# Performance work log

Hardware: AMD Instinct MI355X
Metric: run time of the kernel (lower is better)

Reference implementation:

```python
import jax, jax.numpy as jnp
import numpy as np

LAMBDA_BOX = 1.0
LAMBDA_OBJ = 1.0
IOU_THRESHOLD = 0.2
ALPHA = 0.25
GAMMA = 2.0
EPS = 1e-7  # torchvision complete_box_iou_loss eps


def box_cxcywh_to_xyxy(boxes):
    # boxes [..., 4] (cx, cy, w, h); w,h clamped to min 1e-4 as in the torch code
    cx, cy, w, h = jnp.split(boxes, 4, axis=-1)
    w = jnp.maximum(w, 1e-4)
    h = jnp.maximum(h, 1e-4)
    return jnp.concatenate([cx - w / 2, cy - h / 2, cx + w / 2, cy + h / 2], axis=-1)


def pairwise_box_iou(a, b):
    # a [B,N,4] xyxy, b [B,M,4] xyxy -> [B,N,M] (torchvision box_iou: inter/union, no eps)
    a = a[:, :, None, :]  # [B,N,1,4]
    b = b[:, None, :, :]  # [B,1,M,4]
    lt = jnp.maximum(a[..., :2], b[..., :2])
    rb = jnp.minimum(a[..., 2:], b[..., 2:])
    wh = jnp.clip(rb - lt, 0.0)
    inter = wh[..., 0] * wh[..., 1]
    area_a = (a[..., 2] - a[..., 0]) * (a[..., 3] - a[..., 1])
    area_b = (b[..., 2] - b[..., 0]) * (b[..., 3] - b[..., 1])
    return inter / (area_a + area_b - inter)


def ciou_loss(p, t):
    # torchvision.ops.complete_box_iou_loss, elementwise over [...,4] xyxy boxes
    x1p, y1p, x2p, y2p = p[..., 0], p[..., 1], p[..., 2], p[..., 3]
    x1t, y1t, x2t, y2t = t[..., 0], t[..., 1], t[..., 2], t[..., 3]
    lt_x = jnp.maximum(x1p, x1t); lt_y = jnp.maximum(y1p, y1t)
    rb_x = jnp.minimum(x2p, x2t); rb_y = jnp.minimum(y2p, y2t)
    inter = jnp.clip(rb_x - lt_x, 0.0) * jnp.clip(rb_y - lt_y, 0.0)
    union = (x2p - x1p) * (y2p - y1p) + (x2t - x1t) * (y2t - y1t) - inter
    iou = inter / (union + EPS)
    # smallest enclosing box diagonal
    cx1 = jnp.minimum(x1p, x1t); cy1 = jnp.minimum(y1p, y1t)
    cx2 = jnp.maximum(x2p, x2t); cy2 = jnp.maximum(y2p, y2t)
    diag = (cx2 - cx1) ** 2 + (cy2 - cy1) ** 2 + EPS
    centers = ((x1p + x2p - x1t - x2t) ** 2 + (y1p + y2p - y1t - y2t) ** 2) / 4.0
    diou = 1.0 - iou + centers / diag
    wp = x2p - x1p; hp = y2p - y1p
    wt = x2t - x1t; ht = y2t - y1t
    v = (4.0 / (jnp.pi ** 2)) * (jnp.arctan(wt / ht) - jnp.arctan(wp / hp)) ** 2
    alpha = jax.lax.stop_gradient(v / (1.0 - iou + v + EPS))
    return diou + alpha * v


def focal_loss_mean(logits, targets):
    # mean over last axis; matches torch focal_loss with alpha=0.25, gamma=2
    prob = jax.nn.sigmoid(logits)
    # stable BCE-with-logits
    ce = jnp.clip(logits, 0.0) - logits * targets + jnp.log1p(jnp.exp(-jnp.abs(logits)))
    p_t = prob * targets + (1.0 - prob) * (1.0 - targets)
    alpha_t = ALPHA * targets + (1.0 - ALPHA) * (1.0 - targets)
    p_t = jnp.clip(p_t, 1e-6, 1.0 - 1e-6)
    return (alpha_t * (1.0 - p_t) ** GAMMA * ce).mean(axis=-1)


def greedy_match(iou_nm):
    # iou_nm [N,M]: sequential greedy per-GT matching with conf_target gating
    N = iou_nm.shape[0]
    def step(conf_t, iou_col):
        best = jnp.argmax(iou_col)
        ok = (iou_col[best] > IOU_THRESHOLD) & (conf_t[best] < 0.01)
        conf_t = jnp.where(ok, conf_t.at[best].set(1.0), conf_t)
        return conf_t, (best, ok)
    conf_target, (idx, mask) = jax.lax.scan(step, jnp.zeros((N,), iou_nm.dtype), iou_nm.T)
    return conf_target, idx, mask


def setup_inputs() -> dict:
    key = jax.random.key(0)
    k1, k2, k3, k4, k5 = jax.random.split(key, 5)
    B, N, M = 16, 25000, 64
    # predictions: cx,cy in [0,1], w,h in [0.02,0.3], conf logit ~ N(0,1)
    pcxy = jax.random.uniform(k1, (B, N, 2), jnp.float32)
    pwh = jax.random.uniform(k2, (B, N, 2), jnp.float32, 0.02, 0.3)
    pconf = jax.random.normal(k3, (B, N, 1), jnp.float32)
    preds = jnp.concatenate([pcxy, pwh, pconf], axis=-1)
    # GT boxes in xyxy (as consumed directly by box_iou in the torch code)
    gcxy = jax.random.uniform(k4, (B, M, 2), jnp.float32)
    gwh = jax.random.uniform(k5, (B, M, 2), jnp.float32, 0.02, 0.3)
    targets = box_cxcywh_to_xyxy(jnp.concatenate([gcxy, gwh], axis=-1))
    return {"preds": preds, "targets": targets}


def reference(preds, targets):
    # preds [B,N,5], targets [B,M,4] xyxy -> scalar loss
    pred_xyxy = box_cxcywh_to_xyxy(preds[..., :4])  # [B,N,4]
    pred_conf = preds[..., 4]                        # [B,N]
    # matching indices are non-differentiable (argmax selection)
    iou_m = pairwise_box_iou(jax.lax.stop_gradient(pred_xyxy),
                             jax.lax.stop_gradient(targets))  # [B,N,M]
    conf_target, idx, mask = jax.vmap(greedy_match)(iou_m)  # [B,N], [B,M], [B,M]
    conf_loss = focal_loss_mean(pred_conf, conf_target)      # [B]
    # gather matched pred boxes and compute masked-mean CIoU loss per image
    pb = jnp.take_along_axis(pred_xyxy, idx[..., None], axis=1)  # [B,M,4]
    ciou = ciou_loss(pb, targets)                                # [B,M]
    m = mask.astype(ciou.dtype)
    n_match = m.sum(axis=1)
    box_loss = (ciou * m).sum(axis=1) / jnp.maximum(n_match, 1.0)
    per_image = LAMBDA_OBJ * conf_loss + jnp.where(n_match > 0, LAMBDA_BOX * box_loss, 0.0)
    return per_image.mean()
```

## Files before the change

kernel.cpp:

```cpp
#include <hip/hip_runtime.h>
#include <math.h>

#define BATCH 16
#define NPRED 25000
#define MTGT  64
#define CHUNKS 32
#define PPC   800
#define ABLK  512
#define WAVES (ABLK / 64)
#define PPW   (PPC / WAVES)

#define GMAX_OFF 256
#define WS_ZERO_BYTES (GMAX_OFF + BATCH * MTGT * 8)

__device__ __forceinline__ float focal_term(float x, float t) {
    float prob = 1.0f / (1.0f + expf(-x));
    float ce = fmaxf(x, 0.0f) - x * t + log1pf(expf(-fabsf(x)));
    float p_t = prob * t + (1.0f - prob) * (1.0f - t);
    float alpha_t = 0.25f * t + 0.75f * (1.0f - t);
    p_t = fminf(fmaxf(p_t, 1e-6f), 1.0f - 1e-6f);
    float om = 1.0f - p_t;
    return alpha_t * om * om * ce;
}

__global__ __launch_bounds__(ABLK) void iou_argmax_kernel(
    const float* __restrict__ preds,
    const float* __restrict__ targets,
    unsigned long long* __restrict__ gmax,
    float* __restrict__ focal0)
{
    const int b = blockIdx.y;
    const int chunk = blockIdx.x;
    const int t = threadIdx.x;
    const int lane = t & 63;
    const int w = t >> 6;

    __shared__ float4 sbox[PPC];
    __shared__ unsigned long long comb[WAVES][MTGT];
    __shared__ float sfocal[WAVES];

    float fsum = 0.0f;
    for (int idx = t; idx < PPC; idx += ABLK) {
        int n = chunk * PPC + idx;
        float4 bx;
        if (n < NPRED) {
            const float* p = preds + ((long)b * NPRED + n) * 5;
            float cx = p[0], cy = p[1];
            float wd = fmaxf(p[2], 1e-4f);
            float hh = fmaxf(p[3], 1e-4f);
            bx.x = cx - wd / 2.0f;
            bx.y = cy - hh / 2.0f;
            bx.z = cx + wd / 2.0f;
            bx.w = cy + hh / 2.0f;
            fsum += focal_term(p[4], 0.0f);
        } else {
            bx = make_float4(3e8f, 3e8f, 3e8f, 3e8f);
        }
        sbox[idx] = bx;
    }
    for (int off = 32; off > 0; off >>= 1) fsum += __shfl_down(fsum, off);
    if (lane == 0) sfocal[w] = fsum;

    const float* tg = targets + ((long)b * MTGT + lane) * 4;
    float tx1 = tg[0], ty1 = tg[1], tx2 = tg[2], ty2 = tg[3];
    float ta = (tx2 - tx1) * (ty2 - ty1);

    __syncthreads();

    const int nbase = chunk * PPC + w * PPW;
    float best_i = 0.0f, best_d = 1.0f;
    int best_n = nbase;
#pragma unroll 4
    for (int j = 0; j < PPW; j++) {
        float4 bx = sbox[w * PPW + j];
        float ap = (bx.z - bx.x) * (bx.w - bx.y);
        float ltx = fmaxf(bx.x, tx1), lty = fmaxf(bx.y, ty1);
        float rbx = fminf(bx.z, tx2), rby = fminf(bx.w, ty2);
        float inter = fmaxf(rbx - ltx, 0.0f) * fmaxf(rby - lty, 0.0f);
        float den = ap + ta - inter;
        bool better = (inter * best_d) > (best_i * den);
        best_i = better ? inter : best_i;
        best_d = better ? den : best_d;
        best_n = better ? (nbase + j) : best_n;
    }
    float iou = best_i / best_d;
    comb[w][lane] =
        ((unsigned long long)__float_as_uint(iou) << 32) | (unsigned int)(~best_n);

    __syncthreads();

    if (t < MTGT) {
        unsigned long long v = comb[0][t];
        for (int ww = 1; ww < WAVES; ww++) {
            unsigned long long o = comb[ww][t];
            v = (o > v) ? o : v;
        }
        atomicMax(&gmax[b * MTGT + t], v);
    }
    if (t == 0) {
        float s = 0.0f;
        for (int ww = 0; ww < WAVES; ww++) s += sfocal[ww];
        atomicAdd(&focal0[b], s);
    }
}

__global__ __launch_bounds__(64) void finalize_kernel(
    const float* __restrict__ preds,
    const float* __restrict__ targets,
    const unsigned long long* __restrict__ gmax,
    const float* __restrict__ focal0,
    float* __restrict__ out)
{
    const int b = blockIdx.x;
    const int t = threadIdx.x;

    unsigned long long packed = gmax[b * MTGT + t];
    int id = (int)(~(unsigned int)packed);

    const float* tgp = targets + ((long)b * MTGT + t) * 4;
    float x1t = tgp[0], y1t = tgp[1], x2t = tgp[2], y2t = tgp[3];

    float x1p = 0.f, y1p = 0.f, x2p = 0.f, y2p = 0.f, cf = 0.f;
    float v = 0.0f;
    if (id >= 0 && id < NPRED) {
        const float* p = preds + ((long)b * NPRED + id) * 5;
        float cx = p[0], cy = p[1];
        float wd = fmaxf(p[2], 1e-4f);
        float hh = fmaxf(p[3], 1e-4f);
        cf = p[4];
        x1p = cx - wd / 2.0f; y1p = cy - hh / 2.0f;
        x2p = cx + wd / 2.0f; y2p = cy + hh / 2.0f;
        float ltx = fmaxf(x1p, x1t), lty = fmaxf(y1p, y1t);
        float rbx = fminf(x2p, x2t), rby = fminf(y2p, y2t);
        float inter = fmaxf(rbx - ltx, 0.0f) * fmaxf(rby - lty, 0.0f);
        float ap = (x2p - x1p) * (y2p - y1p);
        float at = (x2t - x1t) * (y2t - y1t);
        v = inter / (ap + at - inter);
    }

    bool accepted = false;
    for (int m = 0; m < MTGT; m++) {
        float vm = __shfl(v, m);
        int im = __shfl(id, m);
        unsigned long long conflict = __ballot(accepted && (id == im));
        bool ok = (vm > 0.2f) && (conflict == 0ull);
        if (t == m) accepted = ok;
    }

    float csum = 0.0f, dsum = 0.0f;
    int cnt = 0;
    if (accepted) {
        float ltx = fmaxf(x1p, x1t), lty = fmaxf(y1p, y1t);
        float rbx = fminf(x2p, x2t), rby = fminf(y2p, y2t);
        float inter = fmaxf(rbx - ltx, 0.0f) * fmaxf(rby - lty, 0.0f);
        float uni = (x2p - x1p) * (y2p - y1p) + (x2t - x1t) * (y2t - y1t) - inter;
        float iou = inter / (uni + 1e-7f);
        float cx1 = fminf(x1p, x1t), cy1 = fminf(y1p, y1t);
        float cx2 = fmaxf(x2p, x2t), cy2 = fmaxf(y2p, y2t);
        float dx = cx2 - cx1, dy = cy2 - cy1;
        float diag = dx * dx + dy * dy + 1e-7f;
        float ex = x1p + x2p - x1t - x2t;
        float ey = y1p + y2p - y1t - y2t;
        float centers = (ex * ex + ey * ey) / 4.0f;
        float diou = 1.0f - iou + centers / diag;
        float wp = x2p - x1p, hp = y2p - y1p;
        float wt = x2t - x1t, ht = y2t - y1t;
        float dat = atanf(wt / ht) - atanf(wp / hp);
        float vv = 0.40528473f * (dat * dat);
        float alpha = vv / (1.0f - iou + vv + 1e-7f);
        csum = diou + alpha * vv;
        cnt = 1;
        dsum = focal_term(cf, 1.0f) - focal_term(cf, 0.0f);
    }

    for (int off = 32; off > 0; off >>= 1) {
        csum += __shfl_down(csum, off);
        dsum += __shfl_down(dsum, off);
        cnt  += __shfl_down(cnt, off);
    }
    if (t == 0) {
        float conf = (focal0[b] + dsum) / (float)NPRED;
        float per = conf;
        if (cnt > 0) per += csum / (float)cnt;
        atomicAdd(out, per * (1.0f / (float)BATCH));
    }
}

extern "C" void kernel_launch(void* const* d_in, const int* in_sizes, int n_in,
                              void* d_out, int out_size, void* d_ws, size_t ws_size,
                              hipStream_t stream) {
    const float* preds = (const float*)d_in[0];
    const float* targets = (const float*)d_in[1];
    float* out = (float*)d_out;

    float* focal0 = (float*)d_ws;
    unsigned long long* gmax = (unsigned long long*)((char*)d_ws + GMAX_OFF);

    hipMemsetAsync(d_out, 0, sizeof(float), stream);
    hipMemsetAsync(d_ws, 0, WS_ZERO_BYTES, stream);

    dim3 gridA(CHUNKS, BATCH);
    iou_argmax_kernel<<<gridA, ABLK, 0, stream>>>(preds, targets, gmax, focal0);
    finalize_kernel<<<BATCH, 64, 0, stream>>>(preds, targets, gmax, focal0, out);
}
```

Before: 87.69 us.

## Replace atomics and memsets with per-chunk partials reduced in single-block finalize

The first kernel now writes per-chunk argmax and focal partial results to the workspace instead of using atomicMax/atomicAdd, so both hipMemsetAsync calls can be removed. The finalize kernel becomes one 1024-thread block that reduces the partials per image and writes the output directly. Chunks are doubled to 64 of 400 predictions each, giving 1024 blocks for more parallelism. The inner IoU loop is also restructured to compare two boxes per step, which shortens the dependent compare chain. In exchange, finalize reads more partial data and all batch work runs on a single block.

```diff
diff --git a/kernel.cpp b/kernel.cpp
--- a/kernel.cpp
+++ b/kernel.cpp
@@ -4,14 +4,13 @@
 #define BATCH 16
 #define NPRED 25000
 #define MTGT  64
-#define CHUNKS 32
-#define PPC   800
+#define CHUNKS 64
+#define PPC   400
 #define ABLK  512
 #define WAVES (ABLK / 64)
 #define PPW   (PPC / WAVES)
 
-#define GMAX_OFF 256
-#define WS_ZERO_BYTES (GMAX_OFF + BATCH * MTGT * 8)
+#define PART_BYTES ((size_t)BATCH * CHUNKS * MTGT * 8)
 
 __device__ __forceinline__ float focal_term(float x, float t) {
     float prob = 1.0f / (1.0f + expf(-x));
@@ -26,8 +25,8 @@
 __global__ __launch_bounds__(ABLK) void iou_argmax_kernel(
     const float* __restrict__ preds,
     const float* __restrict__ targets,
-    unsigned long long* __restrict__ gmax,
-    float* __restrict__ focal0)
+    unsigned long long* __restrict__ part,
+    float* __restrict__ focalp)
 {
     const int b = blockIdx.y;
     const int chunk = blockIdx.x;
@@ -40,8 +39,8 @@
     __shared__ float sfocal[WAVES];
 
     float fsum = 0.0f;
-    for (int idx = t; idx < PPC; idx += ABLK) {
-        int n = chunk * PPC + idx;
+    if (t < PPC) {
+        int n = chunk * PPC + t;
         float4 bx;
         if (n < NPRED) {
             const float* p = preds + ((long)b * NPRED + n) * 5;
@@ -52,11 +51,11 @@
             bx.y = cy - hh / 2.0f;
             bx.z = cx + wd / 2.0f;
             bx.w = cy + hh / 2.0f;
-            fsum += focal_term(p[4], 0.0f);
+            fsum = focal_term(p[4], 0.0f);
         } else {
             bx = make_float4(3e8f, 3e8f, 3e8f, 3e8f);
         }
-        sbox[idx] = bx;
+        sbox[t] = bx;
     }
     for (int off = 32; off > 0; off >>= 1) fsum += __shfl_down(fsum, off);
     if (lane == 0) sfocal[w] = fsum;
@@ -68,56 +67,79 @@
     __syncthreads();
 
     const int nbase = chunk * PPC + w * PPW;
-    float best_i = 0.0f, best_d = 1.0f;
-    int best_n = nbase;
-#pragma unroll 4
-    for (int j = 0; j < PPW; j++) {
-        float4 bx = sbox[w * PPW + j];
-        float ap = (bx.z - bx.x) * (bx.w - bx.y);
-        float ltx = fmaxf(bx.x, tx1), lty = fmaxf(bx.y, ty1);
-        float rbx = fminf(bx.z, tx2), rby = fminf(bx.w, ty2);
-        float inter = fmaxf(rbx - ltx, 0.0f) * fmaxf(rby - lty, 0.0f);
-        float den = ap + ta - inter;
-        bool better = (inter * best_d) > (best_i * den);
-        best_i = better ? inter : best_i;
-        best_d = better ? den : best_d;
-        best_n = better ? (nbase + j) : best_n;
-    }
-    float iou = best_i / best_d;
+    float bi = 0.0f, bd = 1.0f;
+    int bn = nbase;
+#pragma unroll 5
+    for (int j = 0; j < PPW; j += 2) {
+        float4 b0 = sbox[w * PPW + j];
+        float4 b1 = sbox[w * PPW + j + 1];
+
+        float a0 = (b0.z - b0.x) * (b0.w - b0.y);
+        float i0 = fmaxf(fminf(b0.z, tx2) - fmaxf(b0.x, tx1), 0.0f) *
+                   fmaxf(fminf(b0.w, ty2) - fmaxf(b0.y, ty1), 0.0f);
+        float d0 = a0 + ta - i0;
+
+        float a1 = (b1.z - b1.x) * (b1.w - b1.y);
+        float i1 = fmaxf(fminf(b1.z, tx2) - fmaxf(b1.x, tx1), 0.0f) *
+                   fmaxf(fminf(b1.w, ty2) - fmaxf(b1.y, ty1), 0.0f);
+        float d1 = a1 + ta - i1;
+
+        bool w1 = (i1 * d0) > (i0 * d1);
+        float wi = w1 ? i1 : i0;
+        float wd = w1 ? d1 : d0;
+        int wn = nbase + j + (w1 ? 1 : 0);
+
+        bool up = (wi * bd) > (bi * wd);
+        bi = up ? wi : bi;
+        bd = up ? wd : bd;
+        bn = up ? wn : bn;
+    }
+    float iou = bi / bd;
     comb[w][lane] =
-        ((unsigned long long)__float_as_uint(iou) << 32) | (unsigned int)(~best_n);
+        ((unsigned long long)__float_as_uint(iou) << 32) | (unsigned int)(~bn);
 
     __syncthreads();
 
     if (t < MTGT) {
         unsigned long long v = comb[0][t];
+#pragma unroll
         for (int ww = 1; ww < WAVES; ww++) {
             unsigned long long o = comb[ww][t];
             v = (o > v) ? o : v;
         }
-        atomicMax(&gmax[b * MTGT + t], v);
+        part[((long)b * CHUNKS + chunk) * MTGT + t] = v;
     }
     if (t == 0) {
-        float s = 0.0f;
-        for (int ww = 0; ww < WAVES; ww++) s += sfocal[ww];
-        atomicAdd(&focal0[b], s);
-    }
-}
-
-__global__ __launch_bounds__(64) void finalize_kernel(
+        float s = sfocal[0];
+#pragma unroll
+        for (int ww = 1; ww < WAVES; ww++) s += sfocal[ww];
+        focalp[b * CHUNKS + chunk] = s;
+    }
+}
+
+__global__ __launch_bounds__(1024) void finalize_kernel(
     const float* __restrict__ preds,
     const float* __restrict__ targets,
-    const unsigned long long* __restrict__ gmax,
-    const float* __restrict__ focal0,
+    const unsigned long long* __restrict__ part,
+    const float* __restrict__ focalp,
     float* __restrict__ out)
 {
-    const int b = blockIdx.x;
     const int t = threadIdx.x;
-
-    unsigned long long packed = gmax[b * MTGT + t];
-    int id = (int)(~(unsigned int)packed);
-
-    const float* tgp = targets + ((long)b * MTGT + t) * 4;
+    const int b = t >> 6;
+    const int lane = t & 63;
+
+    __shared__ float sper[BATCH];
+
+    unsigned long long best = 0ull;
+    const unsigned long long* pp = part + (long)b * CHUNKS * MTGT + lane;
+#pragma unroll 8
+    for (int c = 0; c < CHUNKS; c++) {
+        unsigned long long v = pp[c * MTGT];
+        best = (v > best) ? v : best;
+    }
+    int id = (int)(~(unsigned int)best);
+
+    const float* tgp = targets + ((long)b * MTGT + lane) * 4;
     float x1t = tgp[0], y1t = tgp[1], x2t = tgp[2], y2t = tgp[3];
 
     float x1p = 0.f, y1p = 0.f, x2p = 0.f, y2p = 0.f, cf = 0.f;
@@ -144,7 +166,7 @@
         int im = __shfl(id, m);
         unsigned long long conflict = __ballot(accepted && (id == im));
         bool ok = (vm > 0.2f) && (conflict == 0ull);
-        if (t == m) accepted = ok;
+        if (lane == m) accepted = ok;
     }
 
     float csum = 0.0f, dsum = 0.0f;
@@ -173,16 +195,26 @@
         dsum = focal_term(cf, 1.0f) - focal_term(cf, 0.0f);
     }
 
+    float fsum = focalp[b * CHUNKS + lane];
+
     for (int off = 32; off > 0; off >>= 1) {
         csum += __shfl_down(csum, off);
         dsum += __shfl_down(dsum, off);
+        fsum += __shfl_down(fsum, off);
         cnt  += __shfl_down(cnt, off);
     }
-    if (t == 0) {
-        float conf = (focal0[b] + dsum) / (float)NPRED;
+    if (lane == 0) {
+        float conf = (fsum + dsum) / (float)NPRED;
         float per = conf;
         if (cnt > 0) per += csum / (float)cnt;
-        atomicAdd(out, per * (1.0f / (float)BATCH));
+        sper[b] = per;
+    }
+    __syncthreads();
+    if (t == 0) {
+        float s = 0.0f;
+#pragma unroll
+        for (int bb = 0; bb < BATCH; bb++) s += sper[bb];
+        out[0] = s * (1.0f / (float)BATCH);
     }
 }
 
@@ -193,13 +225,10 @@
     const float* targets = (const float*)d_in[1];
     float* out = (float*)d_out;
 
-    float* focal0 = (float*)d_ws;
-    unsigned long long* gmax = (unsigned long long*)((char*)d_ws + GMAX_OFF);
-
-    hipMemsetAsync(d_out, 0, sizeof(float), stream);
-    hipMemsetAsync(d_ws, 0, WS_ZERO_BYTES, stream);
+    unsigned long long* part = (unsigned long long*)d_ws;
+    float* focalp = (float*)((char*)d_ws + PART_BYTES);
 
     dim3 gridA(CHUNKS, BATCH);
-    iou_argmax_kernel<<<gridA, ABLK, 0, stream>>>(preds, targets, gmax, focal0);
-    finalize_kernel<<<BATCH, 64, 0, stream>>>(preds, targets, gmax, focal0, out);
-}
+    iou_argmax_kernel<<<gridA, ABLK, 0, stream>>>(preds, targets, part, focalp);
+    finalize_kernel<<<1, 1024, 0, stream>>>(preds, targets, part, focalp, out);
+}
```

Measured after the change: 91.37 us. 4.2% more time.
